# Optimization experiments

Measured on AMD Instinct MI355X. Metric: run time of the kernel, lower is better.

Reference implementation:

```python
import jax, jax.numpy as jnp
import numpy as np

NUM_HEADS = 16
HEAD_DIM = 64
EMBED_DIM = 1024
NEG_INF = -1e9
LENGTHS = np.array([1024, 512, 768, 896, 1024, 640, 384, 896], dtype=np.int32)


def rotate_half(x):
    d = x.shape[-1] // 2
    return jnp.concatenate([-x[..., d:], x[..., :d]], axis=-1)


def setup_inputs() -> dict:
    key = jax.random.key(0)
    ks = jax.random.split(key, 8)
    E, H, Dh = EMBED_DIM, NUM_HEADS, HEAD_DIM
    T = int(LENGTHS.sum())  # 6144 packed tokens
    hidden_states = jax.random.normal(ks[0], (T, E), jnp.float32)
    # RoPE tables: positions restart at 0 for each packed segment
    pos = np.concatenate([np.arange(l) for l in LENGTHS]).astype(np.float32)
    inv_freq = 1.0 / (10000.0 ** (np.arange(0, Dh, 2, dtype=np.float32) / Dh))
    freqs = pos[:, None] * inv_freq[None, :]           # [T, Dh/2]
    emb = np.concatenate([freqs, freqs], axis=-1)       # [T, Dh]
    cos = jnp.asarray(np.cos(emb), jnp.float32)
    sin = jnp.asarray(np.sin(emb), jnp.float32)
    s = 0.02
    Wq = jax.random.normal(ks[1], (E, E), jnp.float32) * s
    Wk = jax.random.normal(ks[2], (E, E), jnp.float32) * s
    Wv = jax.random.normal(ks[3], (E, E), jnp.float32) * s
    Wo = jax.random.normal(ks[4], (E, E), jnp.float32) * s
    bq = jnp.zeros((E,), jnp.float32)
    bv = jnp.zeros((E,), jnp.float32)
    bo = jnp.zeros((E,), jnp.float32)
    return dict(hidden_states=hidden_states, seq_len=jnp.asarray(LENGTHS),
                cos=cos, sin=sin, Wq=Wq, bq=bq, Wk=Wk, Wv=Wv, bv=bv, Wo=Wo, bo=bo)


def reference(hidden_states, seq_len, cos, sin, Wq, bq, Wk, Wv, bv, Wo, bo):
    T, E = hidden_states.shape
    H, Dh = NUM_HEADS, HEAD_DIM
    # q/k/v projections (k_proj has no bias, matching nn.Linear(bias=False))
    q = (hidden_states @ Wq.T + bq).reshape(T, H, Dh)
    k = (hidden_states @ Wk.T).reshape(T, H, Dh)
    v = (hidden_states @ Wv.T + bv).reshape(T, H, Dh)
    # rotary embedding, cos/sin broadcast over heads
    c = cos[:, None, :]
    s = sin[:, None, :]
    q = q * c + rotate_half(q) * s
    k = k * c + rotate_half(k) * s
    # unpack ragged -> padded [B, Lmax, H, Dh] (indices are static wrt data)
    lens = np.asarray(seq_len)
    B = lens.shape[0]
    Lmax = int(lens.max())
    cu = np.concatenate([[0], np.cumsum(lens)])
    pad_idx = cu[:-1, None] + np.arange(Lmax)[None, :]   # [B, Lmax]
    valid = np.arange(Lmax)[None, :] < lens[:, None]     # [B, Lmax]
    pad_idx = np.where(valid, pad_idx, 0)
    qp = q[pad_idx]  # [B, Lmax, H, Dh]
    kp = k[pad_idx]
    vp = v[pad_idx]
    # attention with causal + key-padding mask (equivalent to per-segment loop)
    scores = jnp.einsum('bqhd,bkhd->bhqk', qp, kp) / np.sqrt(Dh).astype(np.float32)
    causal = np.tril(np.ones((Lmax, Lmax), dtype=bool))
    mask = causal[None, None, :, :] & valid[:, None, None, :]
    scores = jnp.where(mask, scores, NEG_INF)
    probs = jax.nn.softmax(scores, axis=-1)
    out = jnp.einsum('bhqk,bkhd->bqhd', probs, vp).reshape(B, Lmax, E)
    # repack padded -> [T, E]
    b_ids = np.repeat(np.arange(B), lens)
    l_ids = np.concatenate([np.arange(l) for l in lens])
    packed = out[b_ids, l_ids]
    return packed @ Wo.T + bo
```

## Files before the change

kernel.cpp:

```cpp
#include <hip/hip_runtime.h>
#include <stdint.h>

typedef __bf16 bf16;
typedef __bf16 bf16x8 __attribute__((ext_vector_type(8)));
typedef __bf16 bf16x4 __attribute__((ext_vector_type(4)));
typedef float f32x4 __attribute__((ext_vector_type(4)));

#define T_TOT 6144
#define E_DIM 1024
#define NHEAD 16

__device__ __forceinline__ void gload16(const void* g, void* l) {
    __builtin_amdgcn_global_load_lds((const __attribute__((address_space(1))) void*)g,
                                     (__attribute__((address_space(3))) void*)l, 16, 0, 0);
}

__global__ __launch_bounds__(256) void cvt_all_kernel(const float* __restrict__ hs,
        const float* __restrict__ wq, const float* __restrict__ wk,
        const float* __restrict__ wv, const float* __restrict__ wo,
        bf16* __restrict__ hsb, bf16* __restrict__ wqb, bf16* __restrict__ wkb,
        bf16* __restrict__ wvb, bf16* __restrict__ wob) {
    const size_t TE = (size_t)T_TOT * E_DIM;
    const size_t EE = (size_t)E_DIM * E_DIM;
    size_t i = ((size_t)blockIdx.x * 256 + threadIdx.x) * 4;
    const float* src; bf16* dst; size_t off;
    if (i < TE)               { src = hs; dst = hsb; off = i; }
    else if (i < TE + EE)     { src = wq; dst = wqb; off = i - TE; }
    else if (i < TE + 2 * EE) { src = wk; dst = wkb; off = i - TE - EE; }
    else if (i < TE + 3 * EE) { src = wv; dst = wvb; off = i - TE - 2 * EE; }
    else                      { src = wo; dst = wob; off = i - TE - 3 * EE; }
    float4 v = *reinterpret_cast<const float4*>(src + off);
    union { bf16 h[4]; uint2 u; } pk;
    pk.h[0] = (bf16)v.x; pk.h[1] = (bf16)v.y; pk.h[2] = (bf16)v.z; pk.h[3] = (bf16)v.w;
    *reinterpret_cast<uint2*>(dst + off) = pk.u;
}

template<int MFRAG>
__device__ __forceinline__ void gemm_body(const bf16* __restrict__ A,
                                          const bf16* __restrict__ BT,
                                          const float* __restrict__ bias,
                                          void* __restrict__ Cout,
                                          bool out_f32, bool rope,
                                          const float* __restrict__ cosb,
                                          const float* __restrict__ sinb,
                                          int bm, int bn, int K) {
    constexpr int BM  = MFRAG * 32;
    constexpr int ACH = BM / 64;
    __shared__ bf16 As[2][BM * 32];
    __shared__ bf16 Bs[2][128 * 32];
    const int tid  = threadIdx.x;
    const int lane = tid & 63;
    const int wid  = tid >> 6;
    const int l15  = lane & 15, l4 = lane >> 4;
    const int wr   = wid >> 1, wc = wid & 1;

    f32x4 acc[MFRAG][4] = {};

    const bf16* Ag = A  + (size_t)bm * BM * K;
    const bf16* Bg = BT + (size_t)bn * 128 * K;

    const int srow = tid >> 2, sc4 = (tid & 3) * 8;

    auto stage = [&](int k0, int buf) {
        #pragma unroll
        for (int j = 0; j < ACH; ++j)
            gload16(Ag + (size_t)(j * 64 + srow) * K + k0 + sc4,
                    &As[buf][(j * 256 + wid * 64) * 8]);
        #pragma unroll
        for (int j = 0; j < 2; ++j)
            gload16(Bg + (size_t)(j * 64 + srow) * K + k0 + sc4,
                    &Bs[buf][(j * 256 + wid * 64) * 8]);
    };

    const int nkt = K / 32;
    stage(0, 0);
    __syncthreads();

    for (int t = 0; t < nkt; ++t) {
        const int cur = t & 1;
        if (t + 1 < nkt) stage((t + 1) * 32, cur ^ 1);

        bf16x8 af[MFRAG], bfr[4];
        #pragma unroll
        for (int m = 0; m < MFRAG; ++m)
            af[m] = *reinterpret_cast<const bf16x8*>(
                &As[cur][(wr * (MFRAG * 16) + m * 16 + l15) * 32 + l4 * 8]);
        #pragma unroll
        for (int n = 0; n < 4; ++n)
            bfr[n] = *reinterpret_cast<const bf16x8*>(
                &Bs[cur][(wc * 64 + n * 16 + l15) * 32 + l4 * 8]);
        #pragma unroll
        for (int m = 0; m < MFRAG; ++m)
            #pragma unroll
            for (int n = 0; n < 4; ++n)
                acc[m][n] = __builtin_amdgcn_mfma_f32_16x16x32_bf16(af[m], bfr[n], acc[m][n], 0, 0, 0);

        __syncthreads();
    }

    const int colb = bn * 128 + wc * 64;
    if (rope) {
        #pragma unroll
        for (int n = 0; n < 2; ++n) {
            const int col_lo = colb + n * 16 + l15;
            const int dlo    = n * 16 + l15;
            const float b_lo = bias ? bias[col_lo] : 0.0f;
            const float b_hi = bias ? bias[col_lo + 32] : 0.0f;
            #pragma unroll
            for (int m = 0; m < MFRAG; ++m) {
                #pragma unroll
                for (int r = 0; r < 4; ++r) {
                    const int t = bm * BM + wr * (MFRAG * 16) + m * 16 + l4 * 4 + r;
                    const float c = cosb[t * 64 + dlo];
                    const float s = sinb[t * 64 + dlo];
                    const float lo = acc[m][n][r] + b_lo;
                    const float hi = acc[m][n + 2][r] + b_hi;
                    bf16* Ob = (bf16*)Cout;
                    Ob[(size_t)t * E_DIM + col_lo]      = (bf16)(lo * c - hi * s);
                    Ob[(size_t)t * E_DIM + col_lo + 32] = (bf16)(hi * c + lo * s);
                }
            }
        }
    } else {
        #pragma unroll
        for (int n = 0; n < 4; ++n) {
            const int col  = colb + n * 16 + l15;
            const float bc = bias ? bias[col] : 0.0f;
            #pragma unroll
            for (int m = 0; m < MFRAG; ++m) {
                const int rowb = bm * BM + wr * (MFRAG * 16) + m * 16 + l4 * 4;
                #pragma unroll
                for (int r = 0; r < 4; ++r) {
                    float val = acc[m][n][r] + bc;
                    if (out_f32)
                        reinterpret_cast<float*>(Cout)[(size_t)(rowb + r) * E_DIM + col] = val;
                    else
                        reinterpret_cast<bf16*>(Cout)[(size_t)(rowb + r) * E_DIM + col] = (bf16)val;
                }
            }
        }
    }
}

__global__ __launch_bounds__(256, 4) void qkv_gemm_kernel(
        const bf16* __restrict__ hsb,
        const bf16* __restrict__ wq, const bf16* __restrict__ wk, const bf16* __restrict__ wv,
        const float* __restrict__ bq, const float* __restrict__ bv,
        const float* __restrict__ cosb, const float* __restrict__ sinb,
        bf16* __restrict__ q, bf16* __restrict__ k, bf16* __restrict__ v) {
    const int b   = blockIdx.x;
    const int swz = (b & 7) * 144 + (b >> 3);
    const int bn  = swz & 7;
    const int bm  = (swz >> 3) % 48;
    const int z   = swz / 384;
    const bf16* W     = (z == 0) ? wq : ((z == 1) ? wk : wv);
    const float* bias = (z == 0) ? bq : ((z == 1) ? nullptr : bv);
    bf16* out         = (z == 0) ? q : ((z == 1) ? k : v);
    gemm_body<4>(hsb, W, bias, out, false, z <= 1, cosb, sinb, bm, bn, E_DIM);
}

__global__ __launch_bounds__(256, 4) void out_gemm_kernel(
        const bf16* __restrict__ attnb, const bf16* __restrict__ wo,
        const float* __restrict__ bo, float* __restrict__ out) {
    const int b   = blockIdx.x;
    const int swz = (b & 7) * 96 + (b >> 3);
    const int bn  = swz & 7;
    const int bm  = swz >> 3;
    gemm_body<2>(attnb, wo, bo, out, true, false, nullptr, nullptr, bm, bn, E_DIM);
}

__global__ __launch_bounds__(256) void transpose_v_kernel(const bf16* __restrict__ v,
                                                          bf16* __restrict__ vt) {
    __shared__ bf16 tile[64][72];
    const int h  = blockIdx.x & 15;
    const int t0 = (blockIdx.x >> 4) * 64;
    const int tid = threadIdx.x;
    #pragma unroll
    for (int i = 0; i < 2; ++i) {
        int c = tid + i * 256;
        int r = c >> 3, c8 = (c & 7) * 8;
        *reinterpret_cast<uint4*>(&tile[r][c8]) =
            *reinterpret_cast<const uint4*>(v + (size_t)(t0 + r) * E_DIM + h * 64 + c8);
    }
    __syncthreads();
    #pragma unroll
    for (int i = 0; i < 2; ++i) {
        int c = tid + i * 256;
        int d = c >> 3, t8 = (c & 7) * 8;
        bf16 tmp[8];
        #pragma unroll
        for (int jj = 0; jj < 8; ++jj) tmp[jj] = tile[t8 + jj][d];
        *reinterpret_cast<uint4*>(vt + (size_t)(h * 64 + d) * T_TOT + t0 + t8) =
            *reinterpret_cast<uint4*>(tmp);
    }
}

__device__ __forceinline__ void stage_kv(const bf16* __restrict__ kp, const bf16* __restrict__ vtp,
                                         bf16* kls, bf16* vls, int tok0, int h,
                                         int wid, int lane) {
    #pragma unroll
    for (int j = 0; j < 2; ++j) {
        const int c   = j * 256 + wid * 64 + lane;
        const int row = c >> 3;
        const int c8s = (c & 7) ^ (row & 7);
        gload16(kp  + (size_t)(tok0 + row) * E_DIM + h * 64 + c8s * 8,
                kls + (size_t)(j * 256 + wid * 64) * 8);
        gload16(vtp + (size_t)(h * 64 + row) * T_TOT + tok0 + c8s * 8,
                vls + (size_t)(j * 256 + wid * 64) * 8);
    }
}

__device__ __forceinline__ int swz(int j, int col8) {
    return j * 64 + ((col8 ^ (j & 7)) << 3);
}

__global__ __launch_bounds__(256, 3) void attn_kernel(const bf16* __restrict__ q,
                                                      const bf16* __restrict__ k,
                                                      const bf16* __restrict__ vt,
                                                      bf16* __restrict__ attn) {
    const int cu[9] = {0, 1024, 1536, 2304, 3200, 4224, 4864, 5248, 6144};
    __shared__ bf16 kls[2][64 * 64];
    __shared__ bf16 vls[2][64 * 64];
    __shared__ bf16 p_lds[4][16][72];
    const int h   = blockIdx.x & 15;
    const int qt  = blockIdx.x >> 4;
    const int tid = threadIdx.x, lane = tid & 63, wid = tid >> 6;
    const int l15 = lane & 15, l4 = lane >> 4;

    const int tq0 = qt * 64;
    int b = 0;
    #pragma unroll
    for (int i = 0; i < 8; ++i) if (tq0 >= cu[i + 1]) b = i + 1;
    const int q0  = tq0 + wid * 16;
    const int p0  = q0 - cu[b];
    const int p0b = tq0 - cu[b];
    const int nkt = (p0b >> 6) + 1;
    const int pq  = p0 + l15;

    bf16x8 qf[2];
    #pragma unroll
    for (int kk = 0; kk < 2; ++kk)
        qf[kk] = *reinterpret_cast<const bf16x8*>(
            q + (size_t)(q0 + l15) * E_DIM + h * 64 + kk * 32 + l4 * 8);

    f32x4 o[4] = {};
    float mcur = -1e30f, lcur = 0.0f;

    stage_kv(k, vt, kls[0], vls[0], cu[b], h, wid, lane);
    __syncthreads();

    for (int kt = 0; kt < nkt; ++kt) {
        const int cur = kt & 1;
        if (kt + 1 < nkt)
            stage_kv(k, vt, kls[cur ^ 1], vls[cur ^ 1], cu[b] + (kt + 1) * 64, h, wid, lane);

        const int j0 = kt * 64;
        const bool diag = (kt == nkt - 1);

        f32x4 s[4] = {};
        #pragma unroll
        for (int nt = 0; nt < 4; ++nt) {
            #pragma unroll
            for (int kk = 0; kk < 2; ++kk) {
                bf16x8 kf = *reinterpret_cast<const bf16x8*>(&kls[cur][swz(nt * 16 + l15, kk * 4 + l4)]);
                s[nt] = __builtin_amdgcn_mfma_f32_16x16x32_bf16(kf, qf[kk], s[nt], 0, 0, 0);
            }
        }

        float tmax = -1e30f;
        #pragma unroll
        for (int nt = 0; nt < 4; ++nt) {
            #pragma unroll
            for (int r = 0; r < 4; ++r) {
                float sv = s[nt][r] * 0.125f;
                if (diag) {
                    const int kp = j0 + nt * 16 + l4 * 4 + r;
                    sv = (kp <= pq) ? sv : -1e30f;
                }
                s[nt][r] = sv;
                tmax = fmaxf(tmax, sv);
            }
        }
        tmax = fmaxf(tmax, __shfl_xor(tmax, 16));
        tmax = fmaxf(tmax, __shfl_xor(tmax, 32));
        const float mnew  = fmaxf(mcur, tmax);
        const float alpha = __expf(mcur - mnew);

        float rs = 0.0f;
        #pragma unroll
        for (int nt = 0; nt < 4; ++nt) {
            bf16x4 pk;
            #pragma unroll
            for (int r = 0; r < 4; ++r) {
                float p = __expf(s[nt][r] - mnew);
                rs += p;
                pk[r] = (bf16)p;
            }
            *reinterpret_cast<bf16x4*>(&p_lds[wid][l15][nt * 16 + l4 * 4]) = pk;
        }
        rs += __shfl_xor(rs, 16);
        rs += __shfl_xor(rs, 32);
        lcur = lcur * alpha + rs;
        mcur = mnew;

        float ar[4];
        #pragma unroll
        for (int r = 0; r < 4; ++r) ar[r] = __shfl(alpha, l4 * 4 + r);
        #pragma unroll
        for (int nt = 0; nt < 4; ++nt)
            #pragma unroll
            for (int r = 0; r < 4; ++r) o[nt][r] *= ar[r];

        bf16x8 pf[2];
        #pragma unroll
        for (int kk = 0; kk < 2; ++kk)
            pf[kk] = *reinterpret_cast<const bf16x8*>(&p_lds[wid][l15][kk * 32 + l4 * 8]);

        #pragma unroll
        for (int nt = 0; nt < 4; ++nt) {
            #pragma unroll
            for (int kk = 0; kk < 2; ++kk) {
                bf16x8 vf = *reinterpret_cast<const bf16x8*>(&vls[cur][swz(nt * 16 + l15, kk * 4 + l4)]);
                o[nt] = __builtin_amdgcn_mfma_f32_16x16x32_bf16(pf[kk], vf, o[nt], 0, 0, 0);
            }
        }
        __syncthreads();
    }

    float rinv[4];
    #pragma unroll
    for (int r = 0; r < 4; ++r)
        rinv[r] = __builtin_amdgcn_rcpf(__shfl(lcur, l4 * 4 + r));
    #pragma unroll
    for (int nt = 0; nt < 4; ++nt) {
        #pragma unroll
        for (int r = 0; r < 4; ++r) {
            float val = o[nt][r] * rinv[r];
            attn[(size_t)(q0 + l4 * 4 + r) * E_DIM + h * 64 + nt * 16 + l15] = (bf16)val;
        }
    }
}

extern "C" void kernel_launch(void* const* d_in, const int* in_sizes, int n_in,
                              void* d_out, int out_size, void* d_ws, size_t ws_size,
                              hipStream_t stream) {
    const float* hs   = (const float*)d_in[0];
    const float* cosb = (const float*)d_in[2];
    const float* sinb = (const float*)d_in[3];
    const float* Wq   = (const float*)d_in[4];
    const float* bq   = (const float*)d_in[5];
    const float* Wk   = (const float*)d_in[6];
    const float* Wv   = (const float*)d_in[7];
    const float* bv   = (const float*)d_in[8];
    const float* Wo   = (const float*)d_in[9];
    const float* bo   = (const float*)d_in[10];

    const size_t TE = (size_t)T_TOT * E_DIM;
    const size_t EE = (size_t)E_DIM * E_DIM;

    char* w = (char*)d_ws;
    bf16* hsb   = (bf16*)w; w += TE * 2;
    bf16* wqb   = (bf16*)w; w += EE * 2;
    bf16* wkb   = (bf16*)w; w += EE * 2;
    bf16* wvb   = (bf16*)w; w += EE * 2;
    bf16* wob   = (bf16*)w; w += EE * 2;
    bf16* qb    = (bf16*)w; w += TE * 2;
    bf16* kb    = (bf16*)w; w += TE * 2;
    bf16* vb    = (bf16*)w; w += TE * 2;
    bf16* vtb   = (bf16*)w; w += TE * 2;
    bf16* attnb = (bf16*)w; w += TE * 2;

    const int cvt_blocks = (int)((TE + 4 * EE) / 4 / 256);
    cvt_all_kernel<<<cvt_blocks, 256, 0, stream>>>(hs, Wq, Wk, Wv, Wo, hsb, wqb, wkb, wvb, wob);

    qkv_gemm_kernel<<<1152, 256, 0, stream>>>(hsb, wqb, wkb, wvb, bq, bv, cosb, sinb, qb, kb, vb);

    transpose_v_kernel<<<(T_TOT / 64) * NHEAD, 256, 0, stream>>>(vb, vtb);

    attn_kernel<<<(T_TOT / 64) * NHEAD, 256, 0, stream>>>(qb, kb, vtb, attnb);

    out_gemm_kernel<<<768, 256, 0, stream>>>(attnb, wob, bo, (float*)d_out);
}
```

Before: 139.7 us.

## Replace QKV GEMM with 256x256-tile 8-wave kernel with swizzled LDS pipeline

Swaps the 128x128-tile QKV projection GEMM for a new kernel that uses 256x256 tiles, 512 threads, K-step 64 with XOR-swizzled LDS, direct global-to-LDS loads and a four-phase ping-pong schedule with setprio around the MFMA bursts. The larger tile raises arithmetic intensity and cuts redundant global traffic. RoPE now exchanges the high half through LDS in the epilogue because the wave layout no longer keeps both halves in one thread. The cost is heavy LDS use (128 KB) and register pressure, and only 288 blocks, which is close to one wave on the device and risks poor tail balance.

```diff
diff --git a/kernel.cpp b/kernel.cpp
--- a/kernel.cpp
+++ b/kernel.cpp
@@ -14,6 +14,9 @@
     __builtin_amdgcn_global_load_lds((const __attribute__((address_space(1))) void*)g,
                                      (__attribute__((address_space(3))) void*)l, 16, 0, 0);
 }
+
+#define BAR() do { __builtin_amdgcn_sched_barrier(0); __builtin_amdgcn_s_barrier(); \
+                   __builtin_amdgcn_sched_barrier(0); } while (0)
 
 __global__ __launch_bounds__(256) void cvt_all_kernel(const float* __restrict__ hs,
         const float* __restrict__ wq, const float* __restrict__ wk,
@@ -35,14 +38,210 @@
     *reinterpret_cast<uint2*>(dst + off) = pk.u;
 }
 
+__global__ __launch_bounds__(512, 2) void qkv256_kernel(
+        const bf16* __restrict__ hsb,
+        const bf16* __restrict__ wq, const bf16* __restrict__ wk, const bf16* __restrict__ wv,
+        const float* __restrict__ bq, const float* __restrict__ bv,
+        const float* __restrict__ cosb, const float* __restrict__ sinb,
+        bf16* __restrict__ qout, bf16* __restrict__ kout, bf16* __restrict__ vout) {
+    __shared__ __align__(16) char smem_raw[131072];
+    bf16* AL = (bf16*)smem_raw;
+    bf16* BL = (bf16*)(smem_raw + 65536);
+    float (*ex)[128] = reinterpret_cast<float(*)[128]>(smem_raw);
+
+    const int bidx  = blockIdx.x;
+    const int swzid = (bidx & 7) * 36 + (bidx >> 3);
+    const int bn = swzid & 3;
+    const int bm = (swzid >> 2) % 24;
+    const int z  = swzid / 96;
+    const bf16*  W    = (z == 0) ? wq : (z == 1) ? wk : wv;
+    const float* bias = (z == 0) ? bq : (z == 1) ? nullptr : bv;
+    bf16*        out  = (z == 0) ? qout : (z == 1) ? kout : vout;
+
+    const int tid  = threadIdx.x;
+    const int lane = tid & 63, wid = tid >> 6;
+    const int l15  = lane & 15, l4 = lane >> 4;
+    const int wr   = wid >> 2, wc = wid & 3;
+    const int l7   = l15 & 7;
+
+    const bf16* Ag = hsb + (size_t)bm * 256 * E_DIM;
+    const bf16* Bg = W   + (size_t)bn * 256 * E_DIM;
+
+    const int srow  = tid >> 3;
+    const int sslot = (tid & 7) ^ (srow & 7);
+    const int ldsoff = wid * 64 * 8;
+
+    auto stA = [&](int tt, int half) {
+        bf16* d = AL + ((tt & 1) * 2 + half) * 8192;
+        const bf16* s = Ag + (size_t)(half * 128 + srow) * E_DIM + tt * 64 + sslot * 8;
+        gload16(s, d + ldsoff);
+        gload16(s + (size_t)64 * E_DIM, d + 4096 + ldsoff);
+    };
+    auto stB = [&](int tt, int half) {
+        bf16* d = BL + ((tt & 1) * 2 + half) * 8192;
+        const bf16* s = Bg + (size_t)(half * 128 + srow) * E_DIM + tt * 64 + sslot * 8;
+        gload16(s, d + ldsoff);
+        gload16(s + (size_t)64 * E_DIM, d + 4096 + ldsoff);
+    };
+
+    const int rA  = wr * 16 + l15;
+    const int rB  = wc * 16 + l15;
+    const int sl0 = (l4) ^ l7;
+    const int sl1 = (4 + l4) ^ l7;
+
+    f32x4 acc[8][4] = {};
+    bf16x8 a0[4][2], a1[4][2], b0[2][2], b1[2][2];
+
+    stA(0, 0); stA(0, 1); stB(0, 0); stB(0, 1);
+    stA(1, 0); stB(1, 1); stA(1, 1);
+    asm volatile("s_waitcnt vmcnt(6)" ::: "memory");
+    BAR();
+
+    const int NT = E_DIM / 64;
+    for (int t = 0; t < NT; ++t) {
+        const int c = t & 1;
+        const bf16* Ab = AL + c * 16384;
+        const bf16* Bb = BL + c * 16384;
+
+        #pragma unroll
+        for (int m = 0; m < 4; ++m) {
+            a0[m][0] = *(const bf16x8*)(Ab + (m * 32 + rA) * 64 + sl0 * 8);
+            a0[m][1] = *(const bf16x8*)(Ab + (m * 32 + rA) * 64 + sl1 * 8);
+        }
+        #pragma unroll
+        for (int n = 0; n < 2; ++n) {
+            b0[n][0] = *(const bf16x8*)(Bb + (n * 64 + rB) * 64 + sl0 * 8);
+            b0[n][1] = *(const bf16x8*)(Bb + (n * 64 + rB) * 64 + sl1 * 8);
+        }
+        if (t + 1 < NT) stB(t + 1, 0);
+        BAR();
+        __builtin_amdgcn_s_setprio(1);
+        #pragma unroll
+        for (int m = 0; m < 4; ++m)
+            #pragma unroll
+            for (int n = 0; n < 2; ++n)
+                #pragma unroll
+                for (int ks = 0; ks < 2; ++ks)
+                    acc[m][n] = __builtin_amdgcn_mfma_f32_16x16x32_bf16(a0[m][ks], b0[n][ks], acc[m][n], 0, 0, 0);
+        __builtin_amdgcn_s_setprio(0);
+        BAR();
+
+        #pragma unroll
+        for (int n = 0; n < 2; ++n) {
+            b1[n][0] = *(const bf16x8*)(Bb + 8192 + (n * 64 + rB) * 64 + sl0 * 8);
+            b1[n][1] = *(const bf16x8*)(Bb + 8192 + (n * 64 + rB) * 64 + sl1 * 8);
+        }
+        if (t + 2 < NT) stA(t + 2, 0);
+        BAR();
+        __builtin_amdgcn_s_setprio(1);
+        #pragma unroll
+        for (int m = 0; m < 4; ++m)
+            #pragma unroll
+            for (int n = 0; n < 2; ++n)
+                #pragma unroll
+                for (int ks = 0; ks < 2; ++ks)
+                    acc[m][n + 2] = __builtin_amdgcn_mfma_f32_16x16x32_bf16(a0[m][ks], b1[n][ks], acc[m][n + 2], 0, 0, 0);
+        __builtin_amdgcn_s_setprio(0);
+        BAR();
+
+        #pragma unroll
+        for (int m = 0; m < 4; ++m) {
+            a1[m][0] = *(const bf16x8*)(Ab + 8192 + (m * 32 + rA) * 64 + sl0 * 8);
+            a1[m][1] = *(const bf16x8*)(Ab + 8192 + (m * 32 + rA) * 64 + sl1 * 8);
+        }
+        if (t + 2 < NT) stB(t + 2, 1);
+        BAR();
+        __builtin_amdgcn_s_setprio(1);
+        #pragma unroll
+        for (int m = 0; m < 4; ++m)
+            #pragma unroll
+            for (int n = 0; n < 2; ++n)
+                #pragma unroll
+                for (int ks = 0; ks < 2; ++ks)
+                    acc[m + 4][n + 2] = __builtin_amdgcn_mfma_f32_16x16x32_bf16(a1[m][ks], b1[n][ks], acc[m + 4][n + 2], 0, 0, 0);
+        __builtin_amdgcn_s_setprio(0);
+        BAR();
+
+        #pragma unroll
+        for (int n = 0; n < 2; ++n) {
+            b0[n][0] = *(const bf16x8*)(Bb + (n * 64 + rB) * 64 + sl0 * 8);
+            b0[n][1] = *(const bf16x8*)(Bb + (n * 64 + rB) * 64 + sl1 * 8);
+        }
+        if (t + 2 < NT) stA(t + 2, 1);
+        if (t < NT - 2)       { asm volatile("s_waitcnt vmcnt(6)" ::: "memory"); }
+        else if (t == NT - 2) { asm volatile("s_waitcnt vmcnt(0)" ::: "memory"); }
+        BAR();
+        __builtin_amdgcn_s_setprio(1);
+        #pragma unroll
+        for (int m = 0; m < 4; ++m)
+            #pragma unroll
+            for (int n = 0; n < 2; ++n)
+                #pragma unroll
+                for (int ks = 0; ks < 2; ++ks)
+                    acc[m + 4][n] = __builtin_amdgcn_mfma_f32_16x16x32_bf16(a1[m][ks], b0[n][ks], acc[m + 4][n], 0, 0, 0);
+        __builtin_amdgcn_s_setprio(0);
+        BAR();
+    }
+
+    __syncthreads();
+    const int rowb = bm * 256;
+    if (z == 2) {
+        #pragma unroll
+        for (int n = 0; n < 4; ++n) {
+            const int col = bn * 256 + n * 64 + wc * 16 + l15;
+            const float bc = bias[col];
+            #pragma unroll
+            for (int m = 0; m < 8; ++m)
+                #pragma unroll
+                for (int r = 0; r < 4; ++r)
+                    out[(size_t)(rowb + m * 32 + wr * 16 + l4 * 4 + r) * E_DIM + col] =
+                        (bf16)(acc[m][n][r] + bc);
+        }
+    } else {
+        if (wc >= 2) {
+            #pragma unroll
+            for (int n = 0; n < 4; ++n) {
+                const int col = bn * 256 + n * 64 + wc * 16 + l15;
+                const float bc = bias ? bias[col] : 0.0f;
+                const int hc = n * 32 + (wc - 2) * 16 + l15;
+                #pragma unroll
+                for (int m = 0; m < 8; ++m)
+                    #pragma unroll
+                    for (int r = 0; r < 4; ++r)
+                        ex[m * 32 + wr * 16 + l4 * 4 + r][hc] = acc[m][n][r] + bc;
+            }
+        }
+        __syncthreads();
+        if (wc < 2) {
+            const int dlo = wc * 16 + l15;
+            #pragma unroll
+            for (int n = 0; n < 4; ++n) {
+                const int col = bn * 256 + n * 64 + dlo;
+                const float bc = bias ? bias[col] : 0.0f;
+                const int hc = n * 32 + dlo;
+                #pragma unroll
+                for (int m = 0; m < 8; ++m) {
+                    #pragma unroll
+                    for (int r = 0; r < 4; ++r) {
+                        const int row = rowb + m * 32 + wr * 16 + l4 * 4 + r;
+                        const float cth = cosb[row * 64 + dlo];
+                        const float sth = sinb[row * 64 + dlo];
+                        const float lo = acc[m][n][r] + bc;
+                        const float hi = ex[m * 32 + wr * 16 + l4 * 4 + r][hc];
+                        out[(size_t)row * E_DIM + col]      = (bf16)(lo * cth - hi * sth);
+                        out[(size_t)row * E_DIM + col + 32] = (bf16)(hi * cth + lo * sth);
+                    }
+                }
+            }
+        }
+    }
+}
+
 template<int MFRAG>
 __device__ __forceinline__ void gemm_body(const bf16* __restrict__ A,
                                           const bf16* __restrict__ BT,
                                           const float* __restrict__ bias,
-                                          void* __restrict__ Cout,
-                                          bool out_f32, bool rope,
-                                          const float* __restrict__ cosb,
-                                          const float* __restrict__ sinb,
+                                          float* __restrict__ Cout,
                                           int bm, int bn, int K) {
     constexpr int BM  = MFRAG * 32;
     constexpr int ACH = BM / 64;
@@ -98,65 +297,18 @@
         __syncthreads();
     }
 
-    const int colb = bn * 128 + wc * 64;
-    if (rope) {
-        #pragma unroll
-        for (int n = 0; n < 2; ++n) {
-            const int col_lo = colb + n * 16 + l15;
-            const int dlo    = n * 16 + l15;
-            const float b_lo = bias ? bias[col_lo] : 0.0f;
-            const float b_hi = bias ? bias[col_lo + 32] : 0.0f;
-            #pragma unroll
-            for (int m = 0; m < MFRAG; ++m) {
-                #pragma unroll
-                for (int r = 0; r < 4; ++r) {
-                    const int t = bm * BM + wr * (MFRAG * 16) + m * 16 + l4 * 4 + r;
-                    const float c = cosb[t * 64 + dlo];
-                    const float s = sinb[t * 64 + dlo];
-                    const float lo = acc[m][n][r] + b_lo;
-                    const float hi = acc[m][n + 2][r] + b_hi;
-                    bf16* Ob = (bf16*)Cout;
-                    Ob[(size_t)t * E_DIM + col_lo]      = (bf16)(lo * c - hi * s);
-                    Ob[(size_t)t * E_DIM + col_lo + 32] = (bf16)(hi * c + lo * s);
-                }
-            }
-        }
-    } else {
-        #pragma unroll
-        for (int n = 0; n < 4; ++n) {
-            const int col  = colb + n * 16 + l15;
-            const float bc = bias ? bias[col] : 0.0f;
-            #pragma unroll
-            for (int m = 0; m < MFRAG; ++m) {
-                const int rowb = bm * BM + wr * (MFRAG * 16) + m * 16 + l4 * 4;
-                #pragma unroll
-                for (int r = 0; r < 4; ++r) {
-                    float val = acc[m][n][r] + bc;
-                    if (out_f32)
-                        reinterpret_cast<float*>(Cout)[(size_t)(rowb + r) * E_DIM + col] = val;
-                    else
-                        reinterpret_cast<bf16*>(Cout)[(size_t)(rowb + r) * E_DIM + col] = (bf16)val;
-                }
-            }
-        }
-    }
-}
-
-__global__ __launch_bounds__(256, 4) void qkv_gemm_kernel(
-        const bf16* __restrict__ hsb,
-        const bf16* __restrict__ wq, const bf16* __restrict__ wk, const bf16* __restrict__ wv,
-        const float* __restrict__ bq, const float* __restrict__ bv,
-        const float* __restrict__ cosb, const float* __restrict__ sinb,
-        bf16* __restrict__ q, bf16* __restrict__ k, bf16* __restrict__ v) {
-    const int b   = blockIdx.x;
-    const int swz = (b & 7) * 144 + (b >> 3);
-    const int bn  = swz & 7;
-    const int bm  = (swz >> 3) % 48;
-    const int z   = swz / 384;
-    const bf16* W     = (z == 0) ? wq : ((z == 1) ? wk : wv);
-    const float* bias = (z == 0) ? bq : ((z == 1) ? nullptr : bv);
-    bf16* out         = (z == 0) ? q : ((z == 1) ? k : v);
-    gemm_body<4>(hsb, W, bias, out, false, z <= 1, cosb, sinb, bm, bn, E_DIM);
+    #pragma unroll
+    for (int n = 0; n < 4; ++n) {
+        const int col  = bn * 128 + wc * 64 + n * 16 + l15;
+        const float bc = bias[col];
+        #pragma unroll
+        for (int m = 0; m < MFRAG; ++m) {
+            const int rowb = bm * BM + wr * (MFRAG * 16) + m * 16 + l4 * 4;
+            #pragma unroll
+            for (int r = 0; r < 4; ++r)
+                Cout[(size_t)(rowb + r) * E_DIM + col] = acc[m][n][r] + bc;
+        }
+    }
 }
 
 __global__ __launch_bounds__(256, 4) void out_gemm_kernel(
@@ -166,7 +318,7 @@
     const int swz = (b & 7) * 96 + (b >> 3);
     const int bn  = swz & 7;
     const int bm  = swz >> 3;
-    gemm_body<2>(attnb, wo, bo, out, true, false, nullptr, nullptr, bm, bn, E_DIM);
+    gemm_body<2>(attnb, wo, bo, out, bm, bn, E_DIM);
 }
 
 __global__ __launch_bounds__(256) void transpose_v_kernel(const bf16* __restrict__ v,
@@ -373,7 +525,7 @@
     const int cvt_blocks = (int)((TE + 4 * EE) / 4 / 256);
     cvt_all_kernel<<<cvt_blocks, 256, 0, stream>>>(hs, Wq, Wk, Wv, Wo, hsb, wqb, wkb, wvb, wob);
 
-    qkv_gemm_kernel<<<1152, 256, 0, stream>>>(hsb, wqb, wkb, wvb, bq, bv, cosb, sinb, qb, kb, vb);
+    qkv256_kernel<<<288, 512, 0, stream>>>(hsb, wqb, wkb, wvb, bq, bv, cosb, sinb, qb, kb, vb);
 
     transpose_v_kernel<<<(T_TOT / 64) * NHEAD, 256, 0, stream>>>(vb, vtb);
 
```

Result: slower. 226.7 us (+62.2%).
